# Performance work log

Measured on AMD Instinct MI355X. Metric: run time of the kernel, lower is better.

## Reference

```python
import jax, jax.numpy as jnp
import numpy as np

B, T, H, L = 64, 512, 768, 9


def _crf_logZ(logits, transitions, seqlen):
    # forward algorithm; state freezes at t >= seqlen (tfa semantics)
    Tn = logits.shape[1]
    alpha0 = logits[:, 0]  # [B,L]
    valid = (jnp.arange(1, Tn)[None, :] < seqlen[:, None]).T  # [T-1,B]
    xs = (jnp.swapaxes(logits[:, 1:], 0, 1), valid)

    def step(alpha, inp):
        logit_t, v = inp
        new = jax.nn.logsumexp(alpha[:, :, None] + transitions[None], axis=1) + logit_t
        return jnp.where(v[:, None], new, alpha), None

    alphaT, _ = jax.lax.scan(step, alpha0, xs)
    return jax.nn.logsumexp(alphaT, axis=1)  # [B]


def _crf_score(logits, transitions, label, seqlen):
    Tn = logits.shape[1]
    seqmask = (jnp.arange(Tn)[None, :] < seqlen[:, None]).astype(logits.dtype)  # [B,T]
    unary = jnp.take_along_axis(logits, label[..., None], axis=2)[..., 0]
    unary = jnp.sum(unary * seqmask, axis=1)
    trans = transitions[label[:, :-1], label[:, 1:]]
    trans = jnp.sum(trans * seqmask[:, 1:], axis=1)
    return unary + trans  # [B]


def _viterbi(logits, transitions, seqlen):
    Tn, Ln = logits.shape[1], logits.shape[2]
    alpha0 = logits[:, 0]
    valid = (jnp.arange(1, Tn)[None, :] < seqlen[:, None]).T  # [T-1,B]
    xs = (jnp.swapaxes(logits[:, 1:], 0, 1), valid)
    idL = jnp.arange(Ln, dtype=jnp.int32)

    def step(alpha, inp):
        logit_t, v = inp
        scores = alpha[:, :, None] + transitions[None]  # [B,L,L]
        new = jnp.max(scores, axis=1) + logit_t
        bp = jnp.argmax(scores, axis=1).astype(jnp.int32)  # [B,L]
        alpha = jnp.where(v[:, None], new, alpha)
        bp = jnp.where(v[:, None], bp, idL[None, :])  # identity bp on padded steps
        return alpha, bp

    alphaT, bps = jax.lax.scan(step, alpha0, xs)  # bps: [T-1,B,L]
    last = jnp.argmax(alphaT, axis=1).astype(jnp.int32)  # [B]

    def back(tag, bp):
        prev = jnp.take_along_axis(bp, tag[:, None], axis=1)[:, 0]
        return prev, tag

    first, rest = jax.lax.scan(back, last, bps, reverse=True)
    tags = jnp.concatenate([first[None], rest], axis=0)  # [T,B]
    return jnp.swapaxes(tags, 0, 1)  # [B,T]


def setup_inputs() -> dict:
    key = jax.random.key(0)
    k = jax.random.split(key, 6)
    x = jax.random.normal(k[0], (B, T, H), dtype=jnp.float32)
    W = jax.random.truncated_normal(k[1], -2.0, 2.0, (H, L), dtype=jnp.float32) * 0.02
    b = jnp.zeros((L,), dtype=jnp.float32)
    lim = float(np.sqrt(6.0 / (L + L)))  # glorot_uniform
    transitions = jax.random.uniform(k[2], (L, L), dtype=jnp.float32, minval=-lim, maxval=lim)
    label = jax.random.randint(k[3], (B, T), 0, L, dtype=jnp.int32)
    seqlen = jax.random.randint(k[4], (B,), 1, T + 1, dtype=jnp.int32)
    mask = jnp.arange(T)[None, :] < seqlen[:, None]
    return {"x": x, "W": W, "b": b, "transitions": transitions, "label": label, "seqlen": seqlen, "mask": mask}


def reference(x, W, b, transitions, label, seqlen, mask):
    logits = jnp.einsum('bth,hl->btl', x, W) + b  # dense_ner
    ll = _crf_score(logits, transitions, label, seqlen) - _crf_logZ(logits, transitions, seqlen)
    loss = jnp.mean(-ll)
    vit = _viterbi(logits, transitions, seqlen)
    seqmask = (jnp.arange(logits.shape[1])[None, :] < seqlen[:, None]).astype(jnp.float32)
    accuracy = jnp.sum((vit == label).astype(jnp.float32) * seqmask) / jnp.sum(seqlen.astype(jnp.float32))
    tp = jnp.sum(((label > 0) & (vit == label)).astype(jnp.float32))
    tn = jnp.sum(((label > 0) & (vit != label)).astype(jnp.float32))
    fp = jnp.sum((mask & (label == 0) & (vit > 0)).astype(jnp.float32))
    return vit, tp, tn, fp, loss, accuracy
```

## Files before the change

### kernel.cpp

```cpp
#include <hip/hip_runtime.h>
#include <stdint.h>
#include <math.h>

#define NB 64
#define BT 512
#define NH 768
#define NL 9
#define KQ 192
#define PBT 528

__device__ __forceinline__ float rlane(float v, int i) {
    return __int_as_float(__builtin_amdgcn_readlane(__float_as_int(v), i));
}

__global__ __launch_bounds__(256) void gemm_kernel(
    const float* __restrict__ x, const float* __restrict__ W,
    const float* __restrict__ bias, float* __restrict__ logits)
{
    __shared__ float part[4][64][12];
    const int lane    = threadIdx.x & 63;
    const int wv      = threadIdx.x >> 6;
    const int rowbase = blockIdx.x * 64;
    const float4* xr = (const float4*)(x + (size_t)(rowbase + lane) * NH + wv * KQ);
    const float*  wq = W + wv * KQ * NL;

    float acc[NL];
#pragma unroll
    for (int l = 0; l < NL; ++l) acc[l] = 0.f;

#pragma unroll 8
    for (int k4 = 0; k4 < KQ / 4; ++k4) {
        const float4 xv = xr[k4];
        const float* wp = wq + k4 * 4 * NL;
#pragma unroll
        for (int l = 0; l < NL; ++l)
            acc[l] = fmaf(xv.x, wp[l],
                     fmaf(xv.y, wp[NL + l],
                     fmaf(xv.z, wp[2 * NL + l],
                     fmaf(xv.w, wp[3 * NL + l], acc[l]))));
    }
#pragma unroll
    for (int l = 0; l < NL; ++l) part[wv][lane][l] = acc[l];
    __syncthreads();
    for (int o = threadIdx.x; o < 64 * NL; o += 256) {
        const int r = o / NL, l = o - r * NL;
        const float s = part[0][r][l] + part[1][r][l] + part[2][r][l] + part[3][r][l];
        logits[(size_t)(rowbase + r) * NL + l] = s + bias[l];
    }
}

__global__ __launch_bounds__(256) void crf_kernel(
    const float* __restrict__ logits, const float* __restrict__ trans,
    const int* __restrict__ label, const int* __restrict__ seqlen,
    float* __restrict__ vit_out, float* __restrict__ stats)
{
    __shared__ __align__(16) float lg_lds[PBT * NL];
    __shared__ float    val_lds[BT * NL];
    __shared__ float    trans_lds[NL * NL];
    __shared__ uint8_t  bp_lds[(BT - 1) * NL];
    __shared__ uint64_t packed_lds[BT - 1];
    __shared__ uint8_t  vit_lds[BT];
    __shared__ float    xw[4][4];

    const int b    = blockIdx.x;
    const int tid  = threadIdx.x;
    const int lane = tid & 63;
    const int wv   = tid >> 6;
    const int sl   = seqlen[b];
    const float* lg  = logits + (size_t)b * BT * NL;
    const int*   lab = label + (size_t)b * BT;

    {
        const float4* src = (const float4*)lg;
        float4* dst = (float4*)lg_lds;
        for (int idx = tid; idx < BT * NL / 4; idx += 256) dst[idx] = src[idx];
        for (int idx = BT * NL + tid; idx < PBT * NL; idx += 256) lg_lds[idx] = 0.f;
        if (tid < NL * NL) trans_lds[tid] = trans[tid];
    }
    __syncthreads();

    if (wv == 0) {
        const int j = lane < NL ? lane : 0;
        float E[NL];
#pragma unroll
        for (int i = 0; i < NL; ++i) E[i] = __expf(trans_lds[i * NL + j]) * 0.125f;
        float A = __expf(lg_lds[j]);
        int lc = 0;
        for (int tb = 1; tb < BT + 8; tb += 8) {
            float P[8];
#pragma unroll
            for (int s = 0; s < 8; ++s) P[s] = __expf(lg_lds[(tb + s) * NL + j]);
#pragma unroll
            for (int s = 0; s < 8; ++s) {
                const int t = tb + s;
                const float r0 = rlane(A, 0), r1 = rlane(A, 1), r2 = rlane(A, 2),
                            r3 = rlane(A, 3), r4 = rlane(A, 4), r5 = rlane(A, 5),
                            r6 = rlane(A, 6), r7 = rlane(A, 7), r8 = rlane(A, 8);
                float p0 = r0 * E[0]; p0 = fmaf(r1, E[1], p0); p0 = fmaf(r2, E[2], p0);
                float p1 = r3 * E[3]; p1 = fmaf(r4, E[4], p1); p1 = fmaf(r5, E[5], p1);
                float p2 = r6 * E[6]; p2 = fmaf(r7, E[7], p2); p2 = fmaf(r8, E[8], p2);
                const float An = ((p0 + p1) + p2) * P[s];
                A = (t < sl) ? An : A;
            }
            const float m = fmaxf(fmaxf(
                fmaxf(fmaxf(rlane(A, 0), rlane(A, 1)), fmaxf(rlane(A, 2), rlane(A, 3))),
                fmaxf(fmaxf(rlane(A, 4), rlane(A, 5)), fmaxf(rlane(A, 6), rlane(A, 7)))),
                rlane(A, 8));
            const int ex = (int)((__float_as_uint(m) >> 23) & 0xFFu) - 126;
            const float sc = __uint_as_float((uint32_t)(127 - ex) << 23);
            A *= sc;
            lc += ex;
        }
        const float sum = ((rlane(A, 0) + rlane(A, 1)) + (rlane(A, 2) + rlane(A, 3))) +
                          ((rlane(A, 4) + rlane(A, 5)) + (rlane(A, 6) + rlane(A, 7))) +
                          rlane(A, 8);
        const float logZ = logf(sum) +
            ((float)lc + 3.0f * (float)(sl - 1)) * 0.6931471805599453f;
        if (lane == 0) stats[b * 8 + 1] = logZ;
    } else if (wv == 1) {
        const int j = lane < NL ? lane : 0;
        float tc[NL];
#pragma unroll
        for (int i = 0; i < NL; ++i) tc[i] = trans_lds[i * NL + j];
        float v = lg_lds[j];
        if (lane < NL) val_lds[j] = v;
        for (int tb = 1; tb < BT + 8; tb += 8) {
            float lv[8];
#pragma unroll
            for (int s = 0; s < 8; ++s) lv[s] = lg_lds[(tb + s) * NL + j];
#pragma unroll
            for (int s = 0; s < 8; ++s) {
                const int t = tb + s;
                const float r0 = rlane(v, 0), r1 = rlane(v, 1), r2 = rlane(v, 2),
                            r3 = rlane(v, 3), r4 = rlane(v, 4), r5 = rlane(v, 5),
                            r6 = rlane(v, 6), r7 = rlane(v, 7), r8 = rlane(v, 8);
                const float c0 = r0 + tc[0], c1 = r1 + tc[1], c2 = r2 + tc[2],
                            c3 = r3 + tc[3], c4 = r4 + tc[4], c5 = r5 + tc[5],
                            c6 = r6 + tc[6], c7 = r7 + tc[7], c8 = r8 + tc[8];
                const float m = fmaxf(fmaxf(fmaxf(fmaxf(c0, c1), c2),
                                            fmaxf(fmaxf(c3, c4), c5)),
                                      fmaxf(fmaxf(c6, c7), c8));
                const float nv = m + lv[s];
                v = (t < sl) ? nv : v;
                if (lane < NL && t < BT) val_lds[t * NL + lane] = v;
            }
        }
        const float r0 = rlane(v, 0), r1 = rlane(v, 1), r2 = rlane(v, 2),
                    r3 = rlane(v, 3), r4 = rlane(v, 4), r5 = rlane(v, 5),
                    r6 = rlane(v, 6), r7 = rlane(v, 7), r8 = rlane(v, 8);
        const float m = fmaxf(fmaxf(fmaxf(fmaxf(r0, r1), r2),
                                    fmaxf(fmaxf(r3, r4), r5)),
                              fmaxf(fmaxf(r6, r7), r8));
        const int last = (r0 == m) ? 0 : (r1 == m) ? 1 : (r2 == m) ? 2 :
                         (r3 == m) ? 3 : (r4 == m) ? 4 : (r5 == m) ? 5 :
                         (r6 == m) ? 6 : (r7 == m) ? 7 : 8;
        if (lane == 0) vit_lds[BT - 1] = (uint8_t)last;
    } else if (wv == 2) {
        float s = 0.f;
        for (int t = lane; t < BT; t += 64) {
            const int lb = lab[t];
            if (t < sl) {
                s += lg_lds[t * NL + lb];
                if (t >= 1) s += trans_lds[lab[t - 1] * NL + lb];
            }
        }
#pragma unroll
        for (int off = 32; off >= 1; off >>= 1) s += __shfl_xor(s, off, 64);
        if (lane == 0) stats[b * 8 + 0] = s;
    }
    __syncthreads();

    for (int idx = tid; idx < (BT - 1) * NL; idx += 256) {
        const int tm1 = idx / NL;
        const int jj  = idx - tm1 * NL;
        const int t   = tm1 + 1;
        int bi;
        if (t >= sl) bi = jj;
        else {
            float best = val_lds[tm1 * NL] + trans_lds[jj];
            bi = 0;
#pragma unroll
            for (int i = 1; i < NL; ++i) {
                const float c = val_lds[tm1 * NL + i] + trans_lds[i * NL + jj];
                if (c > best) { best = c; bi = i; }
            }
        }
        bp_lds[idx] = (uint8_t)bi;
    }
    __syncthreads();

    for (int r = tid; r < BT - 1; r += 256) {
        uint64_t p = 0;
#pragma unroll
        for (int i = 0; i < NL; ++i)
            p |= (uint64_t)bp_lds[r * NL + i] << (4 * i);
        packed_lds[r] = p;
    }
    __syncthreads();

    if (tid == 0) {
        int tag = vit_lds[BT - 1];
        for (int t = BT - 2; t >= 0; --t) {
            const uint64_t row = packed_lds[t];
            tag = (int)((row >> (4 * tag)) & 15u);
            vit_lds[t] = (uint8_t)tag;
        }
    }
    __syncthreads();

    float accv = 0.f, tpv = 0.f, tnv = 0.f, fpv = 0.f;
    for (int t = tid; t < BT; t += 256) {
        const int tg = vit_lds[t];
        const int lb = lab[t];
        const bool msk = t < sl;
        vit_out[(size_t)b * BT + t] = (float)tg;
        if (msk && tg == lb) accv += 1.f;
        if (lb > 0 && tg == lb) tpv += 1.f;
        if (lb > 0 && tg != lb) tnv += 1.f;
        if (msk && lb == 0 && tg > 0) fpv += 1.f;
    }
#pragma unroll
    for (int off = 32; off >= 1; off >>= 1) {
        accv += __shfl_xor(accv, off, 64);
        tpv  += __shfl_xor(tpv,  off, 64);
        tnv  += __shfl_xor(tnv,  off, 64);
        fpv  += __shfl_xor(fpv,  off, 64);
    }
    if (lane == 0) { xw[0][wv] = accv; xw[1][wv] = tpv; xw[2][wv] = tnv; xw[3][wv] = fpv; }
    __syncthreads();
    if (tid == 0) {
        stats[b * 8 + 2] = xw[0][0] + xw[0][1] + xw[0][2] + xw[0][3];
        stats[b * 8 + 3] = xw[1][0] + xw[1][1] + xw[1][2] + xw[1][3];
        stats[b * 8 + 4] = xw[2][0] + xw[2][1] + xw[2][2] + xw[2][3];
        stats[b * 8 + 5] = xw[3][0] + xw[3][1] + xw[3][2] + xw[3][3];
    }
}

__global__ __launch_bounds__(64) void finalize_kernel(
    const float* __restrict__ stats, const int* __restrict__ seqlen,
    float* __restrict__ out)
{
    const int lane = threadIdx.x;
    float score = stats[lane * 8 + 0];
    float logZ  = stats[lane * 8 + 1];
    float accv  = stats[lane * 8 + 2];
    float tpv   = stats[lane * 8 + 3];
    float tnv   = stats[lane * 8 + 4];
    float fpv   = stats[lane * 8 + 5];
    float nll   = logZ - score;
    float slf   = (float)seqlen[lane];
#pragma unroll
    for (int off = 32; off >= 1; off >>= 1) {
        nll  += __shfl_xor(nll,  off, 64);
        accv += __shfl_xor(accv, off, 64);
        tpv  += __shfl_xor(tpv,  off, 64);
        tnv  += __shfl_xor(tnv,  off, 64);
        fpv  += __shfl_xor(fpv,  off, 64);
        slf  += __shfl_xor(slf,  off, 64);
    }
    if (lane == 0) {
        out[NB * BT + 0] = tpv;
        out[NB * BT + 1] = tnv;
        out[NB * BT + 2] = fpv;
        out[NB * BT + 3] = nll / (float)NB;
        out[NB * BT + 4] = accv / slf;
    }
}

extern "C" void kernel_launch(void* const* d_in, const int* in_sizes, int n_in,
                              void* d_out, int out_size, void* d_ws, size_t ws_size,
                              hipStream_t stream)
{
    const float* x      = (const float*)d_in[0];
    const float* W      = (const float*)d_in[1];
    const float* bias   = (const float*)d_in[2];
    const float* trans  = (const float*)d_in[3];
    const int*   label  = (const int*)d_in[4];
    const int*   seqlen = (const int*)d_in[5];

    float* out    = (float*)d_out;
    float* logits = (float*)d_ws;
    float* stats  = logits + (size_t)NB * BT * NL;

    gemm_kernel<<<NB * BT / 64, 256, 0, stream>>>(x, W, bias, logits);
    crf_kernel<<<NB, 256, 0, stream>>>(logits, trans, label, seqlen, out, stats);
    finalize_kernel<<<1, 64, 0, stream>>>(stats, seqlen, out);
}
```

Before: 233.5 us.

## Restructure logits GEMM as persistent wave-per-row with register-resident weights

The logits projection is rewritten so that each wavefront computes a whole row. Each lane keeps its 12x9 slice of W in registers, and x rows are read as fully coalesced float4 loads with the next row prefetched. Partial sums are reduced with cross-lane shuffles instead of an LDS partial-sum buffer and a block barrier. A fixed persistent grid of 768 blocks loops over rows. The cost is about 108 weight registers per lane plus an 81-shuffle reduction for every row, which may limit occupancy.

After: 218.1 us. 6.6% less time.

```diff
diff --git a/kernel.cpp b/kernel.cpp
--- a/kernel.cpp
+++ b/kernel.cpp
@@ -6,46 +6,75 @@
 #define BT 512
 #define NH 768
 #define NL 9
-#define KQ 192
 #define PBT 528
 
 __device__ __forceinline__ float rlane(float v, int i) {
     return __int_as_float(__builtin_amdgcn_readlane(__float_as_int(v), i));
 }
 
-__global__ __launch_bounds__(256) void gemm_kernel(
+__global__ __launch_bounds__(256, 2) void gemm_kernel(
     const float* __restrict__ x, const float* __restrict__ W,
     const float* __restrict__ bias, float* __restrict__ logits)
 {
-    __shared__ float part[4][64][12];
-    const int lane    = threadIdx.x & 63;
-    const int wv      = threadIdx.x >> 6;
-    const int rowbase = blockIdx.x * 64;
-    const float4* xr = (const float4*)(x + (size_t)(rowbase + lane) * NH + wv * KQ);
-    const float*  wq = W + wv * KQ * NL;
-
-    float acc[NL];
-#pragma unroll
-    for (int l = 0; l < NL; ++l) acc[l] = 0.f;
-
-#pragma unroll 8
-    for (int k4 = 0; k4 < KQ / 4; ++k4) {
-        const float4 xv = xr[k4];
-        const float* wp = wq + k4 * 4 * NL;
-#pragma unroll
-        for (int l = 0; l < NL; ++l)
-            acc[l] = fmaf(xv.x, wp[l],
-                     fmaf(xv.y, wp[NL + l],
-                     fmaf(xv.z, wp[2 * NL + l],
-                     fmaf(xv.w, wp[3 * NL + l], acc[l]))));
-    }
-#pragma unroll
-    for (int l = 0; l < NL; ++l) part[wv][lane][l] = acc[l];
-    __syncthreads();
-    for (int o = threadIdx.x; o < 64 * NL; o += 256) {
-        const int r = o / NL, l = o - r * NL;
-        const float s = part[0][r][l] + part[1][r][l] + part[2][r][l] + part[3][r][l];
-        logits[(size_t)(rowbase + r) * NL + l] = s + bias[l];
+    const int lane   = threadIdx.x & 63;
+    const int gwave  = (blockIdx.x * blockDim.x + threadIdx.x) >> 6;
+    const int nw     = (gridDim.x * blockDim.x) >> 6;
+
+    float wr[3][4][NL];
+#pragma unroll
+    for (int k = 0; k < 3; ++k)
+#pragma unroll
+        for (int u = 0; u < 4; ++u) {
+            const int h = k * 256 + lane * 4 + u;
+#pragma unroll
+            for (int l = 0; l < NL; ++l) wr[k][u][l] = W[h * NL + l];
+        }
+    const float bj = bias[lane < NL ? lane : 0];
+
+    const int nrows = NB * BT;
+    int row = gwave;
+    if (row >= nrows) return;
+
+    const float4* xr = (const float4*)(x + (size_t)row * NH);
+    float4 a0 = xr[lane], a1 = xr[64 + lane], a2 = xr[128 + lane];
+
+    while (true) {
+        const int nrow = row + nw;
+        float4 b0, b1, b2;
+        if (nrow < nrows) {
+            const float4* xn = (const float4*)(x + (size_t)nrow * NH);
+            b0 = xn[lane]; b1 = xn[64 + lane]; b2 = xn[128 + lane];
+        }
+
+        float acc[NL];
+#pragma unroll
+        for (int l = 0; l < NL; ++l) {
+            float s = a0.x * wr[0][0][l];
+            s = fmaf(a0.y, wr[0][1][l], s);
+            s = fmaf(a0.z, wr[0][2][l], s);
+            s = fmaf(a0.w, wr[0][3][l], s);
+            s = fmaf(a1.x, wr[1][0][l], s);
+            s = fmaf(a1.y, wr[1][1][l], s);
+            s = fmaf(a1.z, wr[1][2][l], s);
+            s = fmaf(a1.w, wr[1][3][l], s);
+            s = fmaf(a2.x, wr[2][0][l], s);
+            s = fmaf(a2.y, wr[2][1][l], s);
+            s = fmaf(a2.z, wr[2][2][l], s);
+            s = fmaf(a2.w, wr[2][3][l], s);
+            acc[l] = s;
+        }
+#pragma unroll
+        for (int off = 32; off >= 1; off >>= 1)
+#pragma unroll
+            for (int l = 0; l < NL; ++l) acc[l] += __shfl_xor(acc[l], off, 64);
+        float outv = acc[0];
+#pragma unroll
+        for (int l = 1; l < NL; ++l) outv = (lane == l) ? acc[l] : outv;
+        if (lane < NL) logits[(size_t)row * NL + lane] = outv + bj;
+
+        row = nrow;
+        if (row >= nrows) break;
+        a0 = b0; a1 = b1; a2 = b2;
     }
 }
 
@@ -282,7 +311,7 @@
     float* logits = (float*)d_ws;
     float* stats  = logits + (size_t)NB * BT * NL;
 
-    gemm_kernel<<<NB * BT / 64, 256, 0, stream>>>(x, W, bias, logits);
+    gemm_kernel<<<768, 256, 0, stream>>>(x, W, bias, logits);
     crf_kernel<<<NB, 256, 0, stream>>>(logits, trans, label, seqlen, out, stats);
     finalize_kernel<<<1, 64, 0, stream>>>(stats, seqlen, out);
 }
```
